# Kernel optimization log

Measured on AMD Instinct MI355X. Metric: run time of the kernel, lower is better.

Reference implementation:

```python
import jax, jax.numpy as jnp
import numpy as np

N_HEADS = 16
SEG_LEN = 512
MSG_LEN = 1536
T_TOTAL = SEG_LEN + MSG_LEN  # 2048


def _build_mask(T):
    # rows < SEG_LEN: attend to all cols < SEG_LEN (full, non-causal block)
    # rows >= SEG_LEN: standard causal (cols <= row)
    rows = jnp.arange(T)[:, None]
    cols = jnp.arange(T)[None, :]
    mask = jnp.where(rows < SEG_LEN, cols < SEG_LEN, cols <= rows)
    return mask  # [T, T] bool


def setup_inputs() -> dict:
    key = jax.random.key(0)
    k1, k2, k3 = jax.random.split(key, 3)
    B, T, E = 4, T_TOTAL, 1024
    x = jax.random.normal(k1, (B, T, E), dtype=jnp.float32)
    W_qkv = jax.random.normal(k2, (E, 3 * E), dtype=jnp.float32) * (1.0 / np.sqrt(E))
    b_qkv = jnp.zeros((3 * E,), dtype=jnp.float32)
    W_proj = jax.random.normal(k3, (E, E), dtype=jnp.float32) * (1.0 / np.sqrt(E))
    b_proj = jnp.zeros((E,), dtype=jnp.float32)
    return {"x": x, "W_qkv": W_qkv, "b_qkv": b_qkv, "W_proj": W_proj, "b_proj": b_proj}


def reference(x, W_qkv, b_qkv, W_proj, b_proj):
    B, T, E = x.shape
    H = N_HEADS
    D = E // H
    qkv = x @ W_qkv + b_qkv  # [B, T, 3E]
    q, k, v = jnp.split(qkv, 3, axis=-1)
    # [B, H, T, D]
    q = q.reshape(B, T, H, D).transpose(0, 2, 1, 3)
    k = k.reshape(B, T, H, D).transpose(0, 2, 1, 3)
    v = v.reshape(B, T, H, D).transpose(0, 2, 1, 3)
    att = jnp.einsum("bhqd,bhkd->bhqk", q, k) * (1.0 / np.sqrt(D))
    mask = _build_mask(T)  # [T, T]
    att = jnp.where(mask[None, None], att, jnp.float32(-jnp.inf))
    att = jax.nn.softmax(att, axis=-1)
    y = jnp.einsum("bhqk,bhkd->bhqd", att, v)
    y = y.transpose(0, 2, 1, 3).reshape(B, T, E)
    return y @ W_proj + b_proj
```

## Files before the change

### kernel.cpp

```cpp
#include <hip/hip_runtime.h>


typedef _Float16 f16;
typedef _Float16 f16x4 __attribute__((ext_vector_type(4)));
typedef _Float16 f16x8 __attribute__((ext_vector_type(8)));
typedef float f32x4 __attribute__((ext_vector_type(4)));

#define MFMA16x32(a, b, c) __builtin_amdgcn_mfma_f32_16x16x32_f16(a, b, c, 0, 0, 0)
#define MFMA16x16(a, b, c) __builtin_amdgcn_mfma_f32_16x16x16f16(a, b, c, 0, 0, 0)

__device__ __forceinline__ void gload_lds16(const void* g, void* l) {
  __builtin_amdgcn_global_load_lds(
      (__attribute__((address_space(1))) void*)g,
      (__attribute__((address_space(3))) void*)l, 16, 0, 0);
}


__global__ void k_cast_f16(const float* __restrict__ x, f16* __restrict__ xh) {
  int i = blockIdx.x * 256 + threadIdx.x;
  float4 v = ((const float4*)x)[i];
  f16x4 o = {(f16)v.x, (f16)v.y, (f16)v.z, (f16)v.w};
  ((f16x4*)xh)[i] = o;
}

__global__ void k_transpose(const float* __restrict__ W, f16* __restrict__ Wt,
                            int Kdim, int Ndim) {
  __shared__ float tile[32][33];
  int n = blockIdx.x * 32 + threadIdx.x;
  int k0 = blockIdx.y * 32;
  for (int j = threadIdx.y; j < 32; j += 8)
    tile[j][threadIdx.x] = W[(size_t)(k0 + j) * Ndim + n];
  __syncthreads();
  int k = k0 + threadIdx.x;
  for (int j = threadIdx.y; j < 32; j += 8)
    Wt[(size_t)(blockIdx.x * 32 + j) * Kdim + k] = (f16)tile[threadIdx.x][j];
}


__global__ __launch_bounds__(256) void k_gemm_qkv(
    const f16* __restrict__ A, const f16* __restrict__ Bt,
    const float* __restrict__ bias,
    f16* __restrict__ Qo, f16* __restrict__ Ko, f16* __restrict__ Vo) {
  constexpr int KD = 1024;
  __shared__ __align__(16) f16 As[128 * 32];
  __shared__ __align__(16) f16 Bs[128 * 32];
  __shared__ __align__(16) f16 Esh[4 * 64 * 72];
  const int tid = threadIdx.x;
  const int wave = tid >> 6, lane = tid & 63;
  const int g = lane >> 4, l16 = lane & 15;
  const int m0 = blockIdx.y * 128, n0 = blockIdx.x * 128;
  const int wm = (wave >> 1) * 64, wn = (wave & 1) * 64;
  const int srow = wave * 16 + (lane >> 2);
  const int skc = (lane & 3) * 8;

  f32x4 acc[4][4] = {};

  for (int k0 = 0; k0 < KD; k0 += 32) {
    __syncthreads();
    for (int it = 0; it < 2; ++it) {
      gload_lds16(A + (size_t)(m0 + it * 64 + srow) * KD + k0 + skc,
                  As + (it * 64 + wave * 16) * 32);
      gload_lds16(Bt + (size_t)(n0 + it * 64 + srow) * KD + k0 + skc,
                  Bs + (it * 64 + wave * 16) * 32);
    }
    __syncthreads();
    f16x8 af[4], bf[4];
    for (int mi = 0; mi < 4; ++mi)
      af[mi] = *(const f16x8*)(As + (wm + mi * 16 + l16) * 32 + g * 8);
    for (int ni = 0; ni < 4; ++ni)
      bf[ni] = *(const f16x8*)(Bs + (wn + ni * 16 + l16) * 32 + g * 8);
    for (int mi = 0; mi < 4; ++mi)
      for (int ni = 0; ni < 4; ++ni)
        acc[mi][ni] = MFMA16x32(af[mi], bf[ni], acc[mi][ni]);
  }

  const int nsub = n0 + wn;
  const int part = nsub >> 10;
  const int h    = (nsub >> 6) & 15;
  const int mg   = m0 + wm;
  const int b    = mg >> 11;
  const int tb   = mg & 2047;
  const size_t bh = (size_t)(b * 16 + h);
  f16* Es = Esh + wave * (64 * 72);

  float bv[4];
  for (int ni = 0; ni < 4; ++ni) bv[ni] = bias[nsub + ni * 16 + l16];

  for (int mi = 0; mi < 4; ++mi)
    for (int ni = 0; ni < 4; ++ni)
      for (int r = 0; r < 4; ++r) {
        f16 hv = (f16)(acc[mi][ni][r] + bv[ni]);
        int mrow = mi * 16 + g * 4 + r, ncol = ni * 16 + l16;
        if (part == 2) Es[ncol * 72 + mrow] = hv;
        else           Es[mrow * 72 + ncol] = hv;
      }

  const int rrow = lane >> 3, rcol = (lane & 7) * 8;
  for (int p = 0; p < 8; ++p) {
    int row = p * 8 + rrow;
    f16x8 vv = *(const f16x8*)(Es + row * 72 + rcol);
    if (part == 0)
      *(f16x8*)(Qo + (bh * 2048 + tb + row) * 64 + rcol) = vv;
    else if (part == 1)
      *(f16x8*)(Ko + (bh * 2048 + tb + row) * 64 + rcol) = vv;
    else
      *(f16x8*)(Vo + (bh * 64 + row) * 2048 + tb + rcol) = vv;
  }
}


__constant__ unsigned char cQA[10] = {15, 14, 13, 12, 11, 10, 9, 8, 7, 5};
__constant__ unsigned char cQB[10] = {255, 255, 255, 255, 0, 1, 2, 3, 6, 4};

__global__ __launch_bounds__(256, 3) void k_attn(
    const f16* __restrict__ Q, const f16* __restrict__ Kb,
    const f16* __restrict__ Vt, f16* __restrict__ Y) {
  __shared__ __align__(16) f16 Ks[2][64 * 64];
  __shared__ __align__(16) f16 Vs[2][64 * 64];
  __shared__ __align__(16) f16 Es[4 * 32 * 72];
  __shared__ float rs[4 * 32];

  const int tid = threadIdx.x;
  const int wave = tid >> 6, lane = tid & 63;
  const int g = lane >> 4, l16 = lane & 15;
  const int bh = blockIdx.y;
  const int b = bh >> 4, h = bh & 15;
  const int srowrel = lane >> 3;
  const int sc = (lane & 7) ^ srowrel;
  const int srw = wave * 8 + srowrel;

  const f32x4 sinit = {-8.65617025f, -8.65617025f, -8.65617025f, -8.65617025f};

  for (int pass = 0; pass < 2; ++pass) {
    const int qt = pass ? (int)cQB[blockIdx.x] : (int)cQA[blockIdx.x];
    if (qt == 255) break;
    const int q0 = qt * 128;
    const int nt = (qt < 4) ? 8 : (qt + 1) * 2;

    f16x8 aq[2][2];
    for (int mi = 0; mi < 2; ++mi) {
      const f16* qrow =
          Q + ((size_t)bh * 2048 + q0 + wave * 32 + mi * 16 + l16) * 64 + g * 8;
      aq[mi][0] = *(const f16x8*)(qrow);
      aq[mi][1] = *(const f16x8*)(qrow + 32);
      for (int kb = 0; kb < 2; ++kb)
        aq[mi][kb] = aq[mi][kb] * (f16)0.18033688f;
    }

    f32x4 o[2][4] = {};
    float rsum[2] = {};

    for (int it = 0; it < 2; ++it) {
      int row = it * 32 + srw;
      gload_lds16(Kb + ((size_t)bh * 2048 + row) * 64 + sc * 8,
                  &Ks[0][(it * 32 + wave * 8) * 64]);
      gload_lds16(Vt + ((size_t)bh * 64 + row) * 2048 + sc * 8,
                  &Vs[0][(it * 32 + wave * 8) * 64]);
    }
    __syncthreads();

    int cur = 0;
    for (int i = 0; i < nt; ++i) {
      if (i + 1 < nt) {
        const int kn0 = (i + 1) << 6;
        for (int it = 0; it < 2; ++it) {
          int row = it * 32 + srw;
          gload_lds16(Kb + ((size_t)bh * 2048 + kn0 + row) * 64 + sc * 8,
                      &Ks[cur ^ 1][(it * 32 + wave * 8) * 64]);
          gload_lds16(Vt + ((size_t)bh * 64 + row) * 2048 + kn0 + sc * 8,
                      &Vs[cur ^ 1][(it * 32 + wave * 8) * 64]);
        }
      }

      const int kt0 = i << 6;
      const f16* Kc = Ks[cur];
      const f16* Vc = Vs[cur];

      f32x4 t[2][4];
      for (int nb = 0; nb < 4; ++nb) {
        int R = nb * 16 + l16, sw = R & 7;
        f16x8 bk0 = *(const f16x8*)(Kc + R * 64 + ((0 + g) ^ sw) * 8);
        f16x8 bk1 = *(const f16x8*)(Kc + R * 64 + ((4 + g) ^ sw) * 8);
        for (int mi = 0; mi < 2; ++mi) {
          f32x4 acc = MFMA16x32(bk0, aq[mi][0], sinit);
          t[mi][nb] = MFMA16x32(bk1, aq[mi][1], acc);
        }
      }

      const bool masked = (q0 >= 512) && (kt0 >= q0);
      f16x4 ap[4][2];
      for (int mi = 0; mi < 2; ++mi) {
        const int mrow = q0 + wave * 32 + mi * 16 + l16;
        for (int nb = 0; nb < 4; ++nb)
          for (int r = 0; r < 4; ++r) {
            float p = __builtin_amdgcn_exp2f(t[mi][nb][r]);
            if (masked && (kt0 + nb * 16 + g * 4 + r > mrow)) p = 0.f;
            rsum[mi] += p;
            ap[nb][mi][r] = (f16)p;
          }
      }

      for (int db = 0; db < 4; ++db)
        for (int nb = 0; nb < 4; ++nb) {
          int R = db * 16 + l16, sw = R & 7;
          int c = nb * 2 + (g >> 1);
          f16x4 bv = *(const f16x4*)(Vc + R * 64 + (c ^ sw) * 8 + (g & 1) * 4);
          for (int mi = 0; mi < 2; ++mi)
            o[mi][db] = MFMA16x16(ap[nb][mi], bv, o[mi][db]);
        }

      __syncthreads();
      cur ^= 1;
    }

    for (int mi = 0; mi < 2; ++mi) {
      rsum[mi] += __shfl_xor(rsum[mi], 16, 64);
      rsum[mi] += __shfl_xor(rsum[mi], 32, 64);
    }

    if (g == 0)
      for (int mi = 0; mi < 2; ++mi) rs[wave * 32 + mi * 16 + l16] = rsum[mi];
    float rinv[2][4];
    for (int mi = 0; mi < 2; ++mi)
      for (int r = 0; r < 4; ++r)
        rinv[mi][r] = 1.0f / rs[wave * 32 + mi * 16 + g * 4 + r];

    f16* Ew = Es + wave * (32 * 72);
    for (int mi = 0; mi < 2; ++mi)
      for (int db = 0; db < 4; ++db)
        for (int r = 0; r < 4; ++r)
          Ew[(mi * 16 + g * 4 + r) * 72 + db * 16 + l16] =
              (f16)(o[mi][db][r] * rinv[mi][r]);

    const int rrow = lane >> 3, rcol = (lane & 7) * 8;
    const size_t ybase = (size_t)b * 2048 + q0 + wave * 32;
    for (int p = 0; p < 4; ++p) {
      int row = p * 8 + rrow;
      f16x8 vv = *(const f16x8*)(Ew + row * 72 + rcol);
      *(f16x8*)(Y + (ybase + row) * 1024 + h * 64 + rcol) = vv;
    }
  }
}


__global__ __launch_bounds__(256) void k_gemm_proj(
    const f16* __restrict__ A, const f16* __restrict__ Bt,
    const float* __restrict__ bias, float* __restrict__ out) {
  constexpr int KD = 1024;
  __shared__ __align__(16) f16 As[128 * 32];
  __shared__ __align__(16) f16 Bs[128 * 32];
  const int tid = threadIdx.x;
  const int wave = tid >> 6, lane = tid & 63;
  const int g = lane >> 4, l16 = lane & 15;
  const int m0 = blockIdx.y * 128, n0 = blockIdx.x * 128;
  const int wm = (wave >> 1) * 64, wn = (wave & 1) * 64;
  const int srow = wave * 16 + (lane >> 2);
  const int skc = (lane & 3) * 8;

  f32x4 acc[4][4] = {};

  for (int k0 = 0; k0 < KD; k0 += 32) {
    __syncthreads();
    for (int it = 0; it < 2; ++it) {
      gload_lds16(A + (size_t)(m0 + it * 64 + srow) * KD + k0 + skc,
                  As + (it * 64 + wave * 16) * 32);
      gload_lds16(Bt + (size_t)(n0 + it * 64 + srow) * KD + k0 + skc,
                  Bs + (it * 64 + wave * 16) * 32);
    }
    __syncthreads();
    f16x8 af[4], bf[4];
    for (int mi = 0; mi < 4; ++mi)
      af[mi] = *(const f16x8*)(As + (wm + mi * 16 + l16) * 32 + g * 8);
    for (int ni = 0; ni < 4; ++ni)
      bf[ni] = *(const f16x8*)(Bs + (wn + ni * 16 + l16) * 32 + g * 8);
    for (int mi = 0; mi < 4; ++mi)
      for (int ni = 0; ni < 4; ++ni)
        acc[mi][ni] = MFMA16x32(af[mi], bf[ni], acc[mi][ni]);
  }

  float bv[4];
  for (int ni = 0; ni < 4; ++ni) bv[ni] = bias[n0 + wn + ni * 16 + l16];

  for (int mi = 0; mi < 4; ++mi)
    for (int ni = 0; ni < 4; ++ni)
      for (int r = 0; r < 4; ++r) {
        int m = m0 + wm + mi * 16 + g * 4 + r;
        int n = n0 + wn + ni * 16 + l16;
        out[(size_t)m * 1024 + n] = acc[mi][ni][r] + bv[ni];
      }
}


extern "C" void kernel_launch(void* const* d_in, const int* in_sizes, int n_in,
                              void* d_out, int out_size, void* d_ws,
                              size_t ws_size, hipStream_t stream) {
  const float* x      = (const float*)d_in[0];
  const float* W_qkv  = (const float*)d_in[1];
  const float* b_qkv  = (const float*)d_in[2];
  const float* W_proj = (const float*)d_in[3];
  const float* b_proj = (const float*)d_in[4];
  float* out = (float*)d_out;

  char* ws = (char*)d_ws;
  f16* xh    = (f16*)ws;   ws += (size_t)8192 * 1024 * 2;
  f16* Wqt   = (f16*)ws;   ws += (size_t)3072 * 1024 * 2;
  f16* Wpt   = (f16*)ws;   ws += (size_t)1024 * 1024 * 2;
  f16* Qb    = (f16*)ws;   ws += (size_t)64 * 2048 * 64 * 2;
  f16* Kb    = (f16*)ws;   ws += (size_t)64 * 2048 * 64 * 2;
  f16* Vt    = (f16*)ws;   ws += (size_t)64 * 64 * 2048 * 2;
  f16* Y = xh;

  k_cast_f16<<<8192, 256, 0, stream>>>(x, xh);
  k_transpose<<<dim3(96, 32), dim3(32, 8), 0, stream>>>(W_qkv, Wqt, 1024, 3072);
  k_transpose<<<dim3(32, 32), dim3(32, 8), 0, stream>>>(W_proj, Wpt, 1024, 1024);
  k_gemm_qkv<<<dim3(24, 64), 256, 0, stream>>>(xh, Wqt, b_qkv, Qb, Kb, Vt);
  k_attn<<<dim3(10, 64), 256, 0, stream>>>(Qb, Kb, Vt, Y);
  k_gemm_proj<<<dim3(8, 64), 256, 0, stream>>>(Y, Wpt, b_proj, out);
}
```

Before: 279.4 us.

## Pair adjacent query tiles per 512-thread attention block; widen GEMM K-step to 64

The attention kernel now runs 8 waves per block, each half handling one of two adjacent query tiles (qa and qa-1). The two halves share a single K/V stream, which is meant to halve K/V global traffic and remove the two-pass constant-table scheduling. Both GEMMs load 64-wide K slices per barrier to cut synchronisation count, and the QKV epilogue reuses the staging LDS with an XOR swizzle instead of a separate padded buffer. The risks are idle waves for the shorter tile on the last K step, more LDS per GEMM block, and changed occupancy.

```diff
diff --git a/kernel.cpp b/kernel.cpp
--- a/kernel.cpp
+++ b/kernel.cpp
@@ -42,36 +42,38 @@
     const float* __restrict__ bias,
     f16* __restrict__ Qo, f16* __restrict__ Ko, f16* __restrict__ Vo) {
   constexpr int KD = 1024;
-  __shared__ __align__(16) f16 As[128 * 32];
-  __shared__ __align__(16) f16 Bs[128 * 32];
-  __shared__ __align__(16) f16 Esh[4 * 64 * 72];
+  __shared__ __align__(16) f16 smem[2 * 128 * 64];
+  f16* As = smem;
+  f16* Bs = smem + 128 * 64;
   const int tid = threadIdx.x;
   const int wave = tid >> 6, lane = tid & 63;
   const int g = lane >> 4, l16 = lane & 15;
   const int m0 = blockIdx.y * 128, n0 = blockIdx.x * 128;
   const int wm = (wave >> 1) * 64, wn = (wave & 1) * 64;
-  const int srow = wave * 16 + (lane >> 2);
-  const int skc = (lane & 3) * 8;
+  const int srow = wave * 8 + (lane >> 3);
+  const int skc = (lane & 7) * 8;
 
   f32x4 acc[4][4] = {};
 
-  for (int k0 = 0; k0 < KD; k0 += 32) {
-    __syncthreads();
-    for (int it = 0; it < 2; ++it) {
-      gload_lds16(A + (size_t)(m0 + it * 64 + srow) * KD + k0 + skc,
-                  As + (it * 64 + wave * 16) * 32);
-      gload_lds16(Bt + (size_t)(n0 + it * 64 + srow) * KD + k0 + skc,
-                  Bs + (it * 64 + wave * 16) * 32);
-    }
-    __syncthreads();
-    f16x8 af[4], bf[4];
-    for (int mi = 0; mi < 4; ++mi)
-      af[mi] = *(const f16x8*)(As + (wm + mi * 16 + l16) * 32 + g * 8);
-    for (int ni = 0; ni < 4; ++ni)
-      bf[ni] = *(const f16x8*)(Bs + (wn + ni * 16 + l16) * 32 + g * 8);
-    for (int mi = 0; mi < 4; ++mi)
+  for (int k0 = 0; k0 < KD; k0 += 64) {
+    __syncthreads();
+    for (int it = 0; it < 4; ++it) {
+      gload_lds16(A + (size_t)(m0 + it * 32 + srow) * KD + k0 + skc,
+                  As + (it * 32 + wave * 8) * 64);
+      gload_lds16(Bt + (size_t)(n0 + it * 32 + srow) * KD + k0 + skc,
+                  Bs + (it * 32 + wave * 8) * 64);
+    }
+    __syncthreads();
+    for (int kk = 0; kk < 64; kk += 32) {
+      f16x8 af[4], bf[4];
+      for (int mi = 0; mi < 4; ++mi)
+        af[mi] = *(const f16x8*)(As + (wm + mi * 16 + l16) * 64 + kk + g * 8);
       for (int ni = 0; ni < 4; ++ni)
-        acc[mi][ni] = MFMA16x32(af[mi], bf[ni], acc[mi][ni]);
+        bf[ni] = *(const f16x8*)(Bs + (wn + ni * 16 + l16) * 64 + kk + g * 8);
+      for (int mi = 0; mi < 4; ++mi)
+        for (int ni = 0; ni < 4; ++ni)
+          acc[mi][ni] = MFMA16x32(af[mi], bf[ni], acc[mi][ni]);
+    }
   }
 
   const int nsub = n0 + wn;
@@ -81,24 +83,29 @@
   const int b    = mg >> 11;
   const int tb   = mg & 2047;
   const size_t bh = (size_t)(b * 16 + h);
-  f16* Es = Esh + wave * (64 * 72);
 
   float bv[4];
   for (int ni = 0; ni < 4; ++ni) bv[ni] = bias[nsub + ni * 16 + l16];
+
+  __syncthreads();
+  f16* Es = smem + wave * 4096;
 
   for (int mi = 0; mi < 4; ++mi)
     for (int ni = 0; ni < 4; ++ni)
       for (int r = 0; r < 4; ++r) {
         f16 hv = (f16)(acc[mi][ni][r] + bv[ni]);
         int mrow = mi * 16 + g * 4 + r, ncol = ni * 16 + l16;
-        if (part == 2) Es[ncol * 72 + mrow] = hv;
-        else           Es[mrow * 72 + ncol] = hv;
+        if (part == 2)
+          Es[ncol * 64 + (mrow ^ ((ncol & 7) << 3))] = hv;
+        else
+          Es[mrow * 64 + (ncol ^ ((mrow & 7) << 3))] = hv;
       }
 
-  const int rrow = lane >> 3, rcol = (lane & 7) * 8;
+  const int rrow = lane >> 3, rj = lane & 7;
   for (int p = 0; p < 8; ++p) {
     int row = p * 8 + rrow;
-    f16x8 vv = *(const f16x8*)(Es + row * 72 + rcol);
+    f16x8 vv = *(const f16x8*)(Es + row * 64 + (rj ^ (row & 7)) * 8);
+    int rcol = rj * 8;
     if (part == 0)
       *(f16x8*)(Qo + (bh * 2048 + tb + row) * 64 + rcol) = vv;
     else if (part == 1)
@@ -109,69 +116,62 @@
 }
 
 
-__constant__ unsigned char cQA[10] = {15, 14, 13, 12, 11, 10, 9, 8, 7, 5};
-__constant__ unsigned char cQB[10] = {255, 255, 255, 255, 0, 1, 2, 3, 6, 4};
-
-__global__ __launch_bounds__(256, 3) void k_attn(
+__global__ __launch_bounds__(512, 4) void k_attn(
     const f16* __restrict__ Q, const f16* __restrict__ Kb,
     const f16* __restrict__ Vt, f16* __restrict__ Y) {
   __shared__ __align__(16) f16 Ks[2][64 * 64];
   __shared__ __align__(16) f16 Vs[2][64 * 64];
-  __shared__ __align__(16) f16 Es[4 * 32 * 72];
-  __shared__ float rs[4 * 32];
+  __shared__ __align__(16) f16 Es[8 * 32 * 72];
+  __shared__ float rs[8 * 32];
 
   const int tid = threadIdx.x;
   const int wave = tid >> 6, lane = tid & 63;
+  const int wlo = wave & 3;
   const int g = lane >> 4, l16 = lane & 15;
-  const int bh = blockIdx.y;
+  const int bh = blockIdx.x;
   const int b = bh >> 4, h = bh & 15;
+  const int p = (blockIdx.x + blockIdx.y) & 7;
+  const int qa = 15 - 2 * p;
+  const int qt = (wave >> 2) ? (qa - 1) : qa;
+  const int q0 = qt * 128;
+  const int ntq = (qt < 4) ? 8 : (qt + 1) * 2;
+  const int nta = (qa < 4) ? 8 : (qa + 1) * 2;
   const int srowrel = lane >> 3;
   const int sc = (lane & 7) ^ srowrel;
   const int srw = wave * 8 + srowrel;
 
   const f32x4 sinit = {-8.65617025f, -8.65617025f, -8.65617025f, -8.65617025f};
 
-  for (int pass = 0; pass < 2; ++pass) {
-    const int qt = pass ? (int)cQB[blockIdx.x] : (int)cQA[blockIdx.x];
-    if (qt == 255) break;
-    const int q0 = qt * 128;
-    const int nt = (qt < 4) ? 8 : (qt + 1) * 2;
-
-    f16x8 aq[2][2];
-    for (int mi = 0; mi < 2; ++mi) {
-      const f16* qrow =
-          Q + ((size_t)bh * 2048 + q0 + wave * 32 + mi * 16 + l16) * 64 + g * 8;
-      aq[mi][0] = *(const f16x8*)(qrow);
-      aq[mi][1] = *(const f16x8*)(qrow + 32);
-      for (int kb = 0; kb < 2; ++kb)
-        aq[mi][kb] = aq[mi][kb] * (f16)0.18033688f;
-    }
-
-    f32x4 o[2][4] = {};
-    float rsum[2] = {};
-
-    for (int it = 0; it < 2; ++it) {
-      int row = it * 32 + srw;
-      gload_lds16(Kb + ((size_t)bh * 2048 + row) * 64 + sc * 8,
-                  &Ks[0][(it * 32 + wave * 8) * 64]);
-      gload_lds16(Vt + ((size_t)bh * 64 + row) * 2048 + sc * 8,
-                  &Vs[0][(it * 32 + wave * 8) * 64]);
-    }
-    __syncthreads();
-
-    int cur = 0;
-    for (int i = 0; i < nt; ++i) {
-      if (i + 1 < nt) {
-        const int kn0 = (i + 1) << 6;
-        for (int it = 0; it < 2; ++it) {
-          int row = it * 32 + srw;
-          gload_lds16(Kb + ((size_t)bh * 2048 + kn0 + row) * 64 + sc * 8,
-                      &Ks[cur ^ 1][(it * 32 + wave * 8) * 64]);
-          gload_lds16(Vt + ((size_t)bh * 64 + row) * 2048 + kn0 + sc * 8,
-                      &Vs[cur ^ 1][(it * 32 + wave * 8) * 64]);
-        }
-      }
-
+  f16x8 aq[2][2];
+  for (int mi = 0; mi < 2; ++mi) {
+    const f16* qrow =
+        Q + ((size_t)bh * 2048 + q0 + wlo * 32 + mi * 16 + l16) * 64 + g * 8;
+    aq[mi][0] = *(const f16x8*)(qrow);
+    aq[mi][1] = *(const f16x8*)(qrow + 32);
+    for (int kb = 0; kb < 2; ++kb)
+      aq[mi][kb] = aq[mi][kb] * (f16)0.18033688f;
+  }
+
+  f32x4 o[2][4] = {};
+  float rsum[2] = {};
+
+  gload_lds16(Kb + ((size_t)bh * 2048 + srw) * 64 + sc * 8,
+              &Ks[0][wave * 8 * 64]);
+  gload_lds16(Vt + ((size_t)bh * 64 + srw) * 2048 + sc * 8,
+              &Vs[0][wave * 8 * 64]);
+  __syncthreads();
+
+  int cur = 0;
+  for (int i = 0; i < nta; ++i) {
+    if (i + 1 < nta) {
+      const int kn0 = (i + 1) << 6;
+      gload_lds16(Kb + ((size_t)bh * 2048 + kn0 + srw) * 64 + sc * 8,
+                  &Ks[cur ^ 1][wave * 8 * 64]);
+      gload_lds16(Vt + ((size_t)bh * 64 + srw) * 2048 + kn0 + sc * 8,
+                  &Vs[cur ^ 1][wave * 8 * 64]);
+    }
+
+    if (i < ntq) {
       const int kt0 = i << 6;
       const f16* Kc = Ks[cur];
       const f16* Vc = Vs[cur];
@@ -190,13 +190,13 @@
       const bool masked = (q0 >= 512) && (kt0 >= q0);
       f16x4 ap[4][2];
       for (int mi = 0; mi < 2; ++mi) {
-        const int mrow = q0 + wave * 32 + mi * 16 + l16;
+        const int mrow = q0 + wlo * 32 + mi * 16 + l16;
         for (int nb = 0; nb < 4; ++nb)
           for (int r = 0; r < 4; ++r) {
-            float p = __builtin_amdgcn_exp2f(t[mi][nb][r]);
-            if (masked && (kt0 + nb * 16 + g * 4 + r > mrow)) p = 0.f;
-            rsum[mi] += p;
-            ap[nb][mi][r] = (f16)p;
+            float pv = __builtin_amdgcn_exp2f(t[mi][nb][r]);
+            if (masked && (kt0 + nb * 16 + g * 4 + r > mrow)) pv = 0.f;
+            rsum[mi] += pv;
+            ap[nb][mi][r] = (f16)pv;
           }
       }
 
@@ -208,37 +208,37 @@
           for (int mi = 0; mi < 2; ++mi)
             o[mi][db] = MFMA16x16(ap[nb][mi], bv, o[mi][db]);
         }
-
-      __syncthreads();
-      cur ^= 1;
-    }
-
-    for (int mi = 0; mi < 2; ++mi) {
-      rsum[mi] += __shfl_xor(rsum[mi], 16, 64);
-      rsum[mi] += __shfl_xor(rsum[mi], 32, 64);
-    }
-
-    if (g == 0)
-      for (int mi = 0; mi < 2; ++mi) rs[wave * 32 + mi * 16 + l16] = rsum[mi];
-    float rinv[2][4];
-    for (int mi = 0; mi < 2; ++mi)
+    }
+
+    __syncthreads();
+    cur ^= 1;
+  }
+
+  for (int mi = 0; mi < 2; ++mi) {
+    rsum[mi] += __shfl_xor(rsum[mi], 16, 64);
+    rsum[mi] += __shfl_xor(rsum[mi], 32, 64);
+  }
+
+  if (g == 0)
+    for (int mi = 0; mi < 2; ++mi) rs[wave * 32 + mi * 16 + l16] = rsum[mi];
+  float rinv[2][4];
+  for (int mi = 0; mi < 2; ++mi)
+    for (int r = 0; r < 4; ++r)
+      rinv[mi][r] = 1.0f / rs[wave * 32 + mi * 16 + g * 4 + r];
+
+  f16* Ew = Es + wave * (32 * 72);
+  for (int mi = 0; mi < 2; ++mi)
+    for (int db = 0; db < 4; ++db)
       for (int r = 0; r < 4; ++r)
-        rinv[mi][r] = 1.0f / rs[wave * 32 + mi * 16 + g * 4 + r];
-
-    f16* Ew = Es + wave * (32 * 72);
-    for (int mi = 0; mi < 2; ++mi)
-      for (int db = 0; db < 4; ++db)
-        for (int r = 0; r < 4; ++r)
-          Ew[(mi * 16 + g * 4 + r) * 72 + db * 16 + l16] =
-              (f16)(o[mi][db][r] * rinv[mi][r]);
-
-    const int rrow = lane >> 3, rcol = (lane & 7) * 8;
-    const size_t ybase = (size_t)b * 2048 + q0 + wave * 32;
-    for (int p = 0; p < 4; ++p) {
-      int row = p * 8 + rrow;
-      f16x8 vv = *(const f16x8*)(Ew + row * 72 + rcol);
-      *(f16x8*)(Y + (ybase + row) * 1024 + h * 64 + rcol) = vv;
-    }
+        Ew[(mi * 16 + g * 4 + r) * 72 + db * 16 + l16] =
+            (f16)(o[mi][db][r] * rinv[mi][r]);
+
+  const int rrow = lane >> 3, rcol = (lane & 7) * 8;
+  const size_t ybase = (size_t)b * 2048 + q0 + wlo * 32;
+  for (int p2 = 0; p2 < 4; ++p2) {
+    int row = p2 * 8 + rrow;
+    f16x8 vv = *(const f16x8*)(Ew + row * 72 + rcol);
+    *(f16x8*)(Y + (ybase + row) * 1024 + h * 64 + rcol) = vv;
   }
 }
 
@@ -247,35 +247,37 @@
     const f16* __restrict__ A, const f16* __restrict__ Bt,
     const float* __restrict__ bias, float* __restrict__ out) {
   constexpr int KD = 1024;
-  __shared__ __align__(16) f16 As[128 * 32];
-  __shared__ __align__(16) f16 Bs[128 * 32];
+  __shared__ __align__(16) f16 As[128 * 64];
+  __shared__ __align__(16) f16 Bs[128 * 64];
   const int tid = threadIdx.x;
   const int wave = tid >> 6, lane = tid & 63;
   const int g = lane >> 4, l16 = lane & 15;
   const int m0 = blockIdx.y * 128, n0 = blockIdx.x * 128;
   const int wm = (wave >> 1) * 64, wn = (wave & 1) * 64;
-  const int srow = wave * 16 + (lane >> 2);
-  const int skc = (lane & 3) * 8;
+  const int srow = wave * 8 + (lane >> 3);
+  const int skc = (lane & 7) * 8;
 
   f32x4 acc[4][4] = {};
 
-  for (int k0 = 0; k0 < KD; k0 += 32) {
-    __syncthreads();
-    for (int it = 0; it < 2; ++it) {
-      gload_lds16(A + (size_t)(m0 + it * 64 + srow) * KD + k0 + skc,
-                  As + (it * 64 + wave * 16) * 32);
-      gload_lds16(Bt + (size_t)(n0 + it * 64 + srow) * KD + k0 + skc,
-                  Bs + (it * 64 + wave * 16) * 32);
-    }
-    __syncthreads();
-    f16x8 af[4], bf[4];
-    for (int mi = 0; mi < 4; ++mi)
-      af[mi] = *(const f16x8*)(As + (wm + mi * 16 + l16) * 32 + g * 8);
-    for (int ni = 0; ni < 4; ++ni)
-      bf[ni] = *(const f16x8*)(Bs + (wn + ni * 16 + l16) * 32 + g * 8);
-    for (int mi = 0; mi < 4; ++mi)
+  for (int k0 = 0; k0 < KD; k0 += 64) {
+    __syncthreads();
+    for (int it = 0; it < 4; ++it) {
+      gload_lds16(A + (size_t)(m0 + it * 32 + srow) * KD + k0 + skc,
+                  As + (it * 32 + wave * 8) * 64);
+      gload_lds16(Bt + (size_t)(n0 + it * 32 + srow) * KD + k0 + skc,
+                  Bs + (it * 32 + wave * 8) * 64);
+    }
+    __syncthreads();
+    for (int kk = 0; kk < 64; kk += 32) {
+      f16x8 af[4], bf[4];
+      for (int mi = 0; mi < 4; ++mi)
+        af[mi] = *(const f16x8*)(As + (wm + mi * 16 + l16) * 64 + kk + g * 8);
       for (int ni = 0; ni < 4; ++ni)
-        acc[mi][ni] = MFMA16x32(af[mi], bf[ni], acc[mi][ni]);
+        bf[ni] = *(const f16x8*)(Bs + (wn + ni * 16 + l16) * 64 + kk + g * 8);
+      for (int mi = 0; mi < 4; ++mi)
+        for (int ni = 0; ni < 4; ++ni)
+          acc[mi][ni] = MFMA16x32(af[mi], bf[ni], acc[mi][ni]);
+    }
   }
 
   float bv[4];
@@ -314,6 +316,6 @@
   k_transpose<<<dim3(96, 32), dim3(32, 8), 0, stream>>>(W_qkv, Wqt, 1024, 3072);
   k_transpose<<<dim3(32, 32), dim3(32, 8), 0, stream>>>(W_proj, Wpt, 1024, 1024);
   k_gemm_qkv<<<dim3(24, 64), 256, 0, stream>>>(xh, Wqt, b_qkv, Qb, Kb, Vt);
-  k_attn<<<dim3(10, 64), 256, 0, stream>>>(Qb, Kb, Vt, Y);
+  k_attn<<<dim3(64, 8), 512, 0, stream>>>(Qb, Kb, Vt, Y);
   k_gemm_proj<<<dim3(8, 64), 256, 0, stream>>>(Y, Wpt, b_proj, out);
 }
```

New measurement: 286.0 us. +2.4%, slower.
